# Kernel optimization log

Hardware: AMD Instinct MI355X
Metric: run time of the kernel (lower is better)

The kernel has to match this reference:

```python
import jax, jax.numpy as jnp
import numpy as np

H, DK, OUT = 8, 32, 256
SQRT_DK = float(np.sqrt(DK))


def _proj(feat, W, b):
    # (N, in) -> (N, H, DK)
    return (feat @ W + b).reshape(feat.shape[0], H, DK)


def _rel(k_src, v_src, q_dst, src, dst, att_w, msg_w, pri, n_dst):
    # HGT-style per-relation edge attention + segment softmax + aggregation.
    key = jnp.einsum('ehd,hdk->ehk', k_src[src], att_w)          # (E,H,DK)
    att = (q_dst[dst] * key).sum(-1) * pri / SQRT_DK             # (E,H)
    val = jnp.einsum('ehd,hdk->ehk', v_src[src], msg_w)          # (E,H,DK)
    m = jax.ops.segment_max(att, dst, num_segments=n_dst)
    m = jnp.where(jnp.isfinite(m), m, 0.0)
    e = jnp.exp(att - m[dst])
    s = jax.ops.segment_sum(e, dst, num_segments=n_dst)
    alpha = e / jnp.maximum(s[dst], 1e-9)
    h = jax.ops.segment_sum(alpha[..., None] * val, dst, num_segments=n_dst)
    return jax.nn.relu(h.reshape(n_dst, OUT))                    # relu per etype (reduce_func)


def _ln(x, g, b):
    mu = x.mean(-1, keepdims=True)
    var = ((x - mu) ** 2).mean(-1, keepdims=True)
    return (x - mu) / jnp.sqrt(var + 1e-5) * g + b


def _forward(feat_word, feat_topic, feat_doc, Wk, bk, Wq, bq, Wv, bv, Wa, ba,
             ln_scale, ln_bias, skip, rel_pri, rel_att, rel_msg,
             src_ww, dst_ww, src_wt, dst_wt, src_wd, dst_wd,
             src_tt, dst_tt, src_td, dst_td):
    # ntype order: word=0, topic=1, doc=2; etype order: ww=0, wt=1, wd=2, tt=3, td=4
    Nw, Nt, Nd = feat_word.shape[0], feat_topic.shape[0], feat_doc.shape[0]
    k_w, q_w, v_w = _proj(feat_word, Wk[0], bk[0]), _proj(feat_word, Wq[0], bq[0]), _proj(feat_word, Wv[0], bv[0])
    k_t, q_t, v_t = _proj(feat_topic, Wk[1], bk[1]), _proj(feat_topic, Wq[1], bq[1]), _proj(feat_topic, Wv[1], bv[1])
    q_d = _proj(feat_doc, Wq[2], bq[2])
    t_ww = _rel(k_w, v_w, q_w, src_ww, dst_ww, rel_att[0], rel_msg[0], rel_pri[0], Nw)
    t_wt = _rel(k_w, v_w, q_t, src_wt, dst_wt, rel_att[1], rel_msg[1], rel_pri[1], Nt)
    t_wd = _rel(k_w, v_w, q_d, src_wd, dst_wd, rel_att[2], rel_msg[2], rel_pri[2], Nd)
    t_tt = _rel(k_t, v_t, q_t, src_tt, dst_tt, rel_att[3], rel_msg[3], rel_pri[3], Nt)
    t_td = _rel(k_t, v_t, q_d, src_td, dst_td, rel_att[4], rel_msg[4], rel_pri[4], Nd)
    # cross_reducer='mean' across etypes targeting each ntype
    t_word, t_topic, t_doc = t_ww, (t_wt + t_tt) * 0.5, (t_wd + t_td) * 0.5
    outs = []
    for i, (t, feat) in enumerate([(t_word, feat_word), (t_topic, feat_topic), (t_doc, feat_doc)]):
        a = jax.nn.sigmoid(skip[i])
        trans = (t @ Wa[i] + ba[i]) * a + feat * (1.0 - a)
        outs.append(_ln(trans, ln_scale[i], ln_bias[i]))
    return jnp.concatenate(outs, axis=0)  # (Nw+Nt+Nd, OUT)


def setup_inputs() -> dict:
    key = jax.random.key(0)
    ks = jax.random.split(key, 32)
    Nw, Nt, Nd, D = 20000, 2000, 5000, 256
    E = {'ww': (150000, Nw, Nw), 'wt': (80000, Nw, Nt), 'wd': (80000, Nw, Nd),
         'tt': (20000, Nt, Nt), 'td': (40000, Nt, Nd)}
    inp = {
        'feat_word': jax.random.normal(ks[0], (Nw, D), jnp.float32),
        'feat_topic': jax.random.normal(ks[1], (Nt, D), jnp.float32),
        'feat_doc': jax.random.normal(ks[2], (Nd, D), jnp.float32),
        'Wk': jax.random.normal(ks[3], (3, D, D), jnp.float32) * 0.05,
        'bk': jax.random.normal(ks[4], (3, D), jnp.float32) * 0.02,
        'Wq': jax.random.normal(ks[5], (3, D, D), jnp.float32) * 0.05,
        'bq': jax.random.normal(ks[6], (3, D), jnp.float32) * 0.02,
        'Wv': jax.random.normal(ks[7], (3, D, D), jnp.float32) * 0.05,
        'bv': jax.random.normal(ks[8], (3, D), jnp.float32) * 0.02,
        'Wa': jax.random.normal(ks[9], (3, D, D), jnp.float32) * 0.05,
        'ba': jax.random.normal(ks[10], (3, D), jnp.float32) * 0.02,
        'ln_scale': jnp.ones((3, D), jnp.float32),
        'ln_bias': jnp.zeros((3, D), jnp.float32),
        'skip': jnp.ones((3,), jnp.float32),
        'rel_pri': jnp.ones((5, H), jnp.float32),
        'rel_att': jax.random.normal(ks[11], (5, H, DK, DK), jnp.float32) * 0.1,
        'rel_msg': jax.random.normal(ks[12], (5, H, DK, DK), jnp.float32) * 0.1,
    }
    for i, (et, (ne, ns, nd)) in enumerate(E.items()):
        inp['src_' + et] = jax.random.randint(ks[13 + 2 * i], (ne,), 0, ns, jnp.int32)
        inp['dst_' + et] = jax.random.randint(ks[14 + 2 * i], (ne,), 0, nd, jnp.int32)
    return inp


def reference(feat_word, feat_topic, feat_doc, Wk, bk, Wq, bq, Wv, bv, Wa, ba,
              ln_scale, ln_bias, skip, rel_pri, rel_att, rel_msg,
              src_ww, dst_ww, src_wt, dst_wt, src_wd, dst_wd,
              src_tt, dst_tt, src_td, dst_td):
    return _forward(feat_word, feat_topic, feat_doc, Wk, bk, Wq, bq, Wv, bv, Wa, ba,
                    ln_scale, ln_bias, skip, rel_pri, rel_att, rel_msg,
                    src_ww, dst_ww, src_wt, dst_wt, src_wd, dst_wd,
                    src_tt, dst_tt, src_td, dst_td)
```

## Files before the change

kernel.cpp:

```cpp
#include <hip/hip_runtime.h>

static constexpr int NW = 20000, NT = 2000, ND = 5000;
static constexpr int E_WW = 150000, E_WT = 80000, E_WD = 80000, E_TT = 20000, E_TD = 40000;

typedef short bf16x8 __attribute__((ext_vector_type(8)));
typedef float f32x4 __attribute__((ext_vector_type(4)));
typedef float f32x2 __attribute__((ext_vector_type(2)));

__device__ __forceinline__ unsigned short f2bf(float f) {
  union { float f; unsigned int u; } c; c.f = f;
  unsigned int u = c.u;
  u += 0x7fffu + ((u >> 16) & 1u);
  return (unsigned short)(u >> 16);
}
__device__ __forceinline__ float bf2f(unsigned short h) {
  union { unsigned int u; float f; } c; c.u = ((unsigned int)h) << 16; return c.f;
}
__device__ __forceinline__ bf16x8 pack8(float4 a, float4 b) {
  bf16x8 r;
  r[0] = (short)f2bf(a.x); r[1] = (short)f2bf(a.y); r[2] = (short)f2bf(a.z); r[3] = (short)f2bf(a.w);
  r[4] = (short)f2bf(b.x); r[5] = (short)f2bf(b.y); r[6] = (short)f2bf(b.z); r[7] = (short)f2bf(b.w);
  return r;
}
__device__ __forceinline__ unsigned char f2fp8(float x) {
  int p = __builtin_amdgcn_cvt_pk_fp8_f32(x, x, 0, false);
  return (unsigned char)(p & 0xff);
}

struct CsrDesc {
  const int* dst[5];
  const int* src[5];
  int E[5], N[5], cbase[5];
};

struct PrepArgs {
  const float* psrc[7]; unsigned short* pdst[7];
  const float* wq[5]; const float* bqp[5];
  unsigned short* qdst[5];
  float* beff;
  const float* att;
  const float* msg; unsigned short* wvp;
  CsrDesc dsc;
  int* counts;
  int bEff, bHw, bHist, bTot;
};
__global__ __launch_bounds__(256) void prep_kernel(PrepArgs a) {
  __shared__ float tile[32][33];
  int b = blockIdx.x;
  int tid = threadIdx.x;
  if (b < a.bEff) {
    int m = b >> 6, bk = ((b >> 3) & 7) * 32, bn = (b & 7) * 32;
    const float* W = a.psrc[m];
    unsigned short* WT = a.pdst[m];
    int tx = tid & 31, ty = tid >> 5;
#pragma unroll
    for (int i = 0; i < 32; i += 8)
      tile[ty + i][tx] = W[(size_t)(bk + ty + i) * 256 + bn + tx];
    __syncthreads();
#pragma unroll
    for (int i = 0; i < 32; i += 8)
      WT[(size_t)(bn + ty + i) * 256 + bk + tx] = f2bf(tile[tx][ty + i]);
  } else if (b < a.bHw) {
    int t = (b - a.bEff) * 256 + tid;
    if (t < 5 * 65536) {
      int r = t >> 16, rem = t & 65535;
      int n = rem >> 8, kk = rem & 255;
      int h = n >> 5, j = n & 31;
      const float* wrow = a.wq[r] + kk * 256 + h * 32;
      const float* arow = a.att + r * 8192 + h * 1024 + j * 32;
      float s = 0.f;
#pragma unroll
      for (int d = 0; d < 32; d += 4) {
        float4 wv = *(const float4*)(wrow + d);
        float4 av = *(const float4*)(arow + d);
        s += wv.x * av.x + wv.y * av.y + wv.z * av.z + wv.w * av.w;
      }
      a.qdst[r][n * 256 + kk] = f2bf(s);
    } else {
      int idx = t - 5 * 65536;
      if (idx < 1280) {
        int r = idx >> 8, n = idx & 255;
        int h = n >> 5, j = n & 31;
        const float* brow = a.bqp[r] + h * 32;
        const float* arow = a.att + r * 8192 + h * 1024 + j * 32;
        float s = 0.f;
#pragma unroll
        for (int d = 0; d < 32; d += 4) {
          float4 bv = *(const float4*)(brow + d);
          float4 av = *(const float4*)(arow + d);
          s += bv.x * av.x + bv.y * av.y + bv.z * av.z + bv.w * av.w;
        }
        a.beff[r * 256 + n] = s;
      }
    }
  } else if (b < a.bHist) {
    int t = (b - a.bHw) * 256 + tid;
    if (t < 5 * 8192) {
      int m = t >> 13, rem = t & 8191;
      int hc = rem >> 9, idx = rem & 511;
      int lane = idx >> 3, j = idx & 7;
      int h = hc >> 1, c = hc & 1;
      int k = (lane >> 4) * 8 + j, n = c * 16 + (lane & 15);
      a.wvp[t] = f2bf(a.msg[(size_t)m * 8192 + h * 1024 + k * 32 + n]);
    }
  } else {
    int t = (b - a.bHist) * 256 + tid;
    int r = 0, base = 0;
    while (r < 5 && t >= base + a.dsc.E[r]) { base += a.dsc.E[r]; r++; }
    if (r >= 5) return;
    int e = t - base;
    atomicAdd(a.counts + a.dsc.cbase[r] + a.dsc.dst[r][e], 1);
  }
}

struct ProjAll {
  const float* A[3];
  const unsigned short* WT[3];
  const float* bias[3][4];
  unsigned char* outB[3][4];
  int esz[3][4];
  int M[3], R[3], C[3], segBase[4];
  const int* counts; int* offsets; int scanN;
};
__global__ __launch_bounds__(256) void proj_all(ProjAll pa) {
  __shared__ unsigned short As[64 * 64];
  __shared__ unsigned short Bs[64 * 64];
  __shared__ int wpart2[4];
  __shared__ int carry2;
  const int tid = threadIdx.x;
  if ((int)blockIdx.x >= pa.segBase[3]) {
    int lane = tid & 63, w = tid >> 6;
    if (tid == 0) carry2 = 0;
    __syncthreads();
    const int N = pa.scanN;
    for (int base = 0; base < N; base += 1024) {
      int idx = base + tid * 4;
      int v0 = 0, v1 = 0, v2 = 0, v3 = 0;
      if (idx + 3 < N) {
        int4 t4 = *(const int4*)(pa.counts + idx);
        v0 = t4.x; v1 = t4.y; v2 = t4.z; v3 = t4.w;
      } else if (idx < N) {
        v0 = pa.counts[idx];
        if (idx + 1 < N) v1 = pa.counts[idx + 1];
        if (idx + 2 < N) v2 = pa.counts[idx + 2];
      }
      int ts = v0 + v1 + v2 + v3;
      int x = ts;
#pragma unroll
      for (int d = 1; d < 64; d <<= 1) {
        int t = __shfl_up(x, d, 64);
        if (lane >= d) x += t;
      }
      if (lane == 63) wpart2[w] = x;
      __syncthreads();
      if (tid == 0) {
        int s = 0;
#pragma unroll
        for (int j = 0; j < 4; j++) { int t = wpart2[j]; wpart2[j] = s; s += t; }
      }
      __syncthreads();
      int excl = carry2 + wpart2[w] + (x - ts);
      if (idx < N)     pa.offsets[idx]     = excl;
      if (idx + 1 < N) pa.offsets[idx + 1] = excl + v0;
      if (idx + 2 < N) pa.offsets[idx + 2] = excl + v0 + v1;
      if (idx + 3 < N) pa.offsets[idx + 3] = excl + v0 + v1 + v2;
      __syncthreads();
      if (tid == 255) carry2 = excl + ts;
      __syncthreads();
    }
    if (tid == 0) pa.offsets[N] = carry2;
    return;
  }
  int nt = 0;
  while (nt < 2 && (int)blockIdx.x >= pa.segBase[nt + 1]) nt++;
  int local = blockIdx.x - pa.segBase[nt];
  const int C = pa.C[nt];
  const int xcd = local & 7, slot = local >> 3;
  const int rt = xcd + 8 * (slot / C);
  const int bnb = slot % C;
  if (rt >= pa.R[nt]) return;
  const int bm = rt * 64, bn = bnb * 64;
  const float* A = pa.A[nt];
  const unsigned short* WT = pa.WT[nt];
  const int M = pa.M[nt];
  const int wave = tid >> 6, lane = tid & 63;
  f32x4 acc[4] = {};
  const int ar = wave * 16 + (lane & 15);
  const int swz = lane & 7;
  for (int k0 = 0; k0 < 256; k0 += 64) {
#pragma unroll
    for (int i = 0; i < 2; i++) {
      int c = tid + i * 256;
      int row = c >> 3, sl = c & 7;
      int srow = bm + row;
      float4 a0 = make_float4(0.f, 0.f, 0.f, 0.f), a1 = a0;
      if (srow < M) {
        a0 = *(const float4*)(A + (size_t)srow * 256 + k0 + sl * 8);
        a1 = *(const float4*)(A + (size_t)srow * 256 + k0 + sl * 8 + 4);
      }
      *(bf16x8*)&As[row * 64 + (sl ^ (row & 7)) * 8] = pack8(a0, a1);
      bf16x8 bv = *(const bf16x8*)(WT + (size_t)(bn + row) * 256 + k0 + sl * 8);
      *(bf16x8*)&Bs[row * 64 + (sl ^ (row & 7)) * 8] = bv;
    }
    __syncthreads();
#pragma unroll
    for (int kk = 0; kk < 2; kk++) {
      int slot2 = kk * 4 + (lane >> 4);
      bf16x8 av = *(const bf16x8*)&As[ar * 64 + ((slot2 ^ swz) * 8)];
#pragma unroll
      for (int nf = 0; nf < 4; nf++) {
        int br = nf * 16 + (lane & 15);
        bf16x8 bv = *(const bf16x8*)&Bs[br * 64 + ((slot2 ^ swz) * 8)];
        acc[nf] = __builtin_amdgcn_mfma_f32_16x16x32_bf16(av, bv, acc[nf], 0, 0, 0);
      }
    }
    __syncthreads();
  }
  const int col = lane & 15;
  const int seg = bnb >> 2;
  const float* bias = pa.bias[nt][seg];
  unsigned char* outB = pa.outB[nt][seg];
  const int esz = pa.esz[nt][seg];
  const int cbase = (bnb & 3) * 64;
#pragma unroll
  for (int nf = 0; nf < 4; nf++) {
    float bsv = bias[cbase + nf * 16 + col];
    int idx = cbase + nf * 16 + col;
#pragma unroll
    for (int rr = 0; rr < 4; rr++) {
      int row = bm + wave * 16 + (lane >> 4) * 4 + rr;
      if (row < M) {
        float v = acc[nf][rr] + bsv;
        if (esz == 2) *(unsigned short*)(outB + (size_t)row * 512 + idx * 2) = f2bf(v);
        else          outB[(size_t)row * 512 + idx] = f2fp8(v);
      }
    }
  }
}

__global__ void scatter5(CsrDesc d, const int* __restrict__ offsets, int* __restrict__ cursor,
                         int* __restrict__ ssrc) {
  int t = blockIdx.x * blockDim.x + threadIdx.x;
  int r = 0, base = 0;
  while (r < 5 && t >= base + d.E[r]) { base += d.E[r]; r++; }
  if (r >= 5) return;
  int e = t - base;
  int dn = d.dst[r][e];
  int pos = offsets[d.cbase[r] + dn] + atomicAdd(cursor + d.cbase[r] + dn, 1);
  ssrc[pos] = d.src[r][e];
}

struct AttArgs {
  const unsigned short* qh[5]; const unsigned char* kv8[5];
  const int* offs[5]; unsigned short* agg[5];
  const int* ssrc;
  const float* pri;
  int bcum[6]; int Ndst[5];
};
__global__ __launch_bounds__(256) void fused_att_agg(AttArgs a) {
  int r = 0;
  while (r < 4 && (int)blockIdx.x >= a.bcum[r + 1]) r++;
  int wave = threadIdx.x >> 6, lane = threadIdx.x & 63;
  int node = (blockIdx.x - a.bcum[r]) * 4 + wave;
  if (node >= a.Ndst[r]) return;
  const unsigned short* qh = a.qh[r];
  const unsigned char* kvb = a.kv8[r];
  const int* ssrc = a.ssrc;
  const int* offs = a.offs[r];
  int h = lane >> 3;
  float prih = a.pri[r * 8 + h] * 0.17677669529663687f;
  int r0 = offs[node], r1 = offs[node + 1];
  float4 acc = make_float4(0.f, 0.f, 0.f, 0.f);
  if (r0 < r1) {
    ushort4 qv = *(const ushort4*)(qh + (size_t)node * 256 + lane * 4);
    float q0 = bf2f(qv.x), q1 = bf2f(qv.y), q2 = bf2f(qv.z), q3 = bf2f(qv.w);
    float m = -1e30f, s = 0.f;
    for (int i = r0; i < r1; i += 2) {
      int sA = ssrc[i];
      bool two = (i + 1 < r1);
      int sB = two ? ssrc[i + 1] : sA;
      const unsigned char* pA = kvb + (size_t)sA * 512 + lane * 4;
      const unsigned char* pB = kvb + (size_t)sB * 512 + lane * 4;
      unsigned int kuA = *(const unsigned int*)pA;
      unsigned int kuB = *(const unsigned int*)pB;
      unsigned int vuA = *(const unsigned int*)(pA + 256);
      unsigned int vuB = *(const unsigned int*)(pB + 256);
      f32x2 ka01 = __builtin_amdgcn_cvt_pk_f32_fp8((int)kuA, false);
      f32x2 ka23 = __builtin_amdgcn_cvt_pk_f32_fp8((int)kuA, true);
      f32x2 kb01 = __builtin_amdgcn_cvt_pk_f32_fp8((int)kuB, false);
      f32x2 kb23 = __builtin_amdgcn_cvt_pk_f32_fp8((int)kuB, true);
      float dA = q0 * ka01[0] + q1 * ka01[1] + q2 * ka23[0] + q3 * ka23[1];
      float dB = q0 * kb01[0] + q1 * kb01[1] + q2 * kb23[0] + q3 * kb23[1];
      dA += __shfl_xor(dA, 1, 64); dB += __shfl_xor(dB, 1, 64);
      dA += __shfl_xor(dA, 2, 64); dB += __shfl_xor(dB, 2, 64);
      dA += __shfl_xor(dA, 4, 64); dB += __shfl_xor(dB, 4, 64);
      float lA = dA * prih;
      float lB = two ? dB * prih : -1e30f;
      float mn = fmaxf(m, fmaxf(lA, lB));
      float sc = __expf(m - mn);
      float wA = __expf(lA - mn);
      float wB = __expf(lB - mn);
      m = mn;
      s = s * sc + wA + wB;
      f32x2 va01 = __builtin_amdgcn_cvt_pk_f32_fp8((int)vuA, false);
      f32x2 va23 = __builtin_amdgcn_cvt_pk_f32_fp8((int)vuA, true);
      f32x2 vb01 = __builtin_amdgcn_cvt_pk_f32_fp8((int)vuB, false);
      f32x2 vb23 = __builtin_amdgcn_cvt_pk_f32_fp8((int)vuB, true);
      acc.x = acc.x * sc + wA * va01[0] + wB * vb01[0];
      acc.y = acc.y * sc + wA * va01[1] + wB * vb01[1];
      acc.z = acc.z * sc + wA * va23[0] + wB * vb23[0];
      acc.w = acc.w * sc + wA * va23[1] + wB * vb23[1];
    }
    float inv = 1.f / fmaxf(s, 1e-9f);
    acc.x *= inv; acc.y *= inv; acc.z *= inv; acc.w *= inv;
  }
  ushort4 o;
  o.x = f2bf(acc.x); o.y = f2bf(acc.y); o.z = f2bf(acc.z); o.w = f2bf(acc.w);
  *(ushort4*)(a.agg[r] + (size_t)node * 256 + lane * 4) = o;
}

struct MsgArgs {
  const unsigned short* aggA[3]; const unsigned short* aggB[3];
  const unsigned short* fA[3]; const unsigned short* fB[3];
  unsigned short* t[3];
  float scale[3];
  int N[3]; int bcum[4];
};
__global__ __launch_bounds__(256) void msg_transform_all(MsgArgs a) {
  int g = 0;
  while (g < 2 && (int)blockIdx.x >= a.bcum[g + 1]) g++;
  int local = blockIdx.x - a.bcum[g];
  const unsigned short* aggA = a.aggA[g];
  const unsigned short* aggB = a.aggB[g];
  const unsigned short* fA = a.fA[g];
  const unsigned short* fB = a.fB[g];
  unsigned short* t = a.t[g];
  float scale = a.scale[g];
  int N = a.N[g];
  int wave = threadIdx.x >> 6, lane = threadIdx.x & 63;
  int r0 = local * 64 + wave * 16;
  int arow = r0 + (lane & 15);
  bool valid = arow < N;
  int kofs = (lane >> 4) * 8;
  f32x4 z{};
#pragma unroll
  for (int h = 0; h < 8; h++) {
    bf16x8 aA{}, aB{};
    if (valid) {
      aA = *(const bf16x8*)(aggA + (size_t)arow * 256 + h * 32 + kofs);
      if (aggB) aB = *(const bf16x8*)(aggB + (size_t)arow * 256 + h * 32 + kofs);
    }
#pragma unroll
    for (int c = 0; c < 2; c++) {
      bf16x8 bA = *(const bf16x8*)(fA + ((h * 2 + c) * 64 + lane) * 8);
      f32x4 oA = __builtin_amdgcn_mfma_f32_16x16x32_bf16(aA, bA, z, 0, 0, 0);
      f32x4 oB = z;
      if (aggB) {
        bf16x8 bB = *(const bf16x8*)(fB + ((h * 2 + c) * 64 + lane) * 8);
        oB = __builtin_amdgcn_mfma_f32_16x16x32_bf16(aB, bB, z, 0, 0, 0);
      }
      int colc = h * 32 + c * 16 + (lane & 15);
#pragma unroll
      for (int rr = 0; rr < 4; rr++) {
        int row = r0 + (lane >> 4) * 4 + rr;
        if (row < N) {
          float v = fmaxf(oA[rr], 0.f) + fmaxf(oB[rr], 0.f);
          t[(size_t)row * 256 + colc] = f2bf(v * scale);
        }
      }
    }
  }
}

struct OutAll {
  const unsigned short* tA[3]; const unsigned short* WT[3];
  const float* ba[3]; const float* feat[3];
  const float* gamma[3]; const float* beta[3];
  float* op[3];
  int M[3], bcum[4];
  const float* skipv;
};
__global__ __launch_bounds__(256) void out_all_ln(OutAll oa) {
  __shared__ unsigned short As[64 * 64];
  __shared__ unsigned short Bs[256 * 64];
  int g = 0;
  while (g < 2 && (int)blockIdx.x >= oa.bcum[g + 1]) g++;
  const int bm = (blockIdx.x - oa.bcum[g]) * 64;
  const unsigned short* tA = oa.tA[g];
  const unsigned short* WT = oa.WT[g];
  const int M = oa.M[g];
  const int tid = threadIdx.x, wave = tid >> 6, lane = tid & 63;
  f32x4 acc[16] = {};
  const int ar = wave * 16 + (lane & 15);
  const int swz = lane & 7;
  for (int k0 = 0; k0 < 256; k0 += 64) {
#pragma unroll
    for (int i = 0; i < 2; i++) {
      int c = tid + i * 256;
      int row = c >> 3, sl = c & 7;
      int srow = bm + row;
      bf16x8 av{};
      if (srow < M) av = *(const bf16x8*)(tA + (size_t)srow * 256 + k0 + sl * 8);
      *(bf16x8*)&As[row * 64 + (sl ^ (row & 7)) * 8] = av;
    }
#pragma unroll
    for (int i = 0; i < 8; i++) {
      int c = tid + i * 256;
      int row = c >> 3, sl = c & 7;
      bf16x8 bv = *(const bf16x8*)(WT + (size_t)row * 256 + k0 + sl * 8);
      *(bf16x8*)&Bs[row * 64 + (sl ^ (row & 7)) * 8] = bv;
    }
    __syncthreads();
#pragma unroll
    for (int kk = 0; kk < 2; kk++) {
      int slot = kk * 4 + (lane >> 4);
      bf16x8 av = *(const bf16x8*)&As[ar * 64 + ((slot ^ swz) * 8)];
#pragma unroll
      for (int nf = 0; nf < 16; nf++) {
        int br = nf * 16 + (lane & 15);
        bf16x8 bv = *(const bf16x8*)&Bs[br * 64 + ((slot ^ swz) * 8)];
        acc[nf] = __builtin_amdgcn_mfma_f32_16x16x32_bf16(av, bv, acc[nf], 0, 0, 0);
      }
    }
    __syncthreads();
  }
  const int c16 = lane & 15;
  float a_skip = 1.f / (1.f + __expf(-oa.skipv[g]));
  float one_m = 1.f - a_skip;
  const float* gamma = oa.gamma[g];
  const float* beta = oa.beta[g];
  const float* ba = oa.ba[g];
  const float* feat = oa.feat[g];
  float* outp = oa.op[g];
  float gg[16], bb[16], bia[16];
#pragma unroll
  for (int nf = 0; nf < 16; nf++) {
    gg[nf] = gamma[nf * 16 + c16];
    bb[nf] = beta[nf * 16 + c16];
    bia[nf] = ba[nf * 16 + c16];
  }
#pragma unroll
  for (int rr = 0; rr < 4; rr++) {
    int row = bm + wave * 16 + (lane >> 4) * 4 + rr;
    bool valid = row < M;
#pragma unroll
    for (int nf = 0; nf < 16; nf++) {
      float fv = valid ? feat[(size_t)row * 256 + nf * 16 + c16] : 0.f;
      acc[nf][rr] = (acc[nf][rr] + bia[nf]) * a_skip + fv * one_m;
    }
    float p = 0.f;
#pragma unroll
    for (int nf = 0; nf < 16; nf++) p += acc[nf][rr];
    p += __shfl_xor(p, 1, 16); p += __shfl_xor(p, 2, 16);
    p += __shfl_xor(p, 4, 16); p += __shfl_xor(p, 8, 16);
    float mu = p * (1.f / 256.f);
    float qv = 0.f;
#pragma unroll
    for (int nf = 0; nf < 16; nf++) { float dd = acc[nf][rr] - mu; qv += dd * dd; }
    qv += __shfl_xor(qv, 1, 16); qv += __shfl_xor(qv, 2, 16);
    qv += __shfl_xor(qv, 4, 16); qv += __shfl_xor(qv, 8, 16);
    float rstd = rsqrtf(qv * (1.f / 256.f) + 1e-5f);
    if (valid) {
#pragma unroll
      for (int nf = 0; nf < 16; nf++)
        outp[(size_t)row * 256 + nf * 16 + c16] = (acc[nf][rr] - mu) * rstd * gg[nf] + bb[nf];
    }
  }
}

extern "C" void kernel_launch(void* const* d_in, const int* in_sizes, int n_in,
                              void* d_out, int out_size, void* d_ws, size_t ws_size,
                              hipStream_t stream) {
  const float* feat_w = (const float*)d_in[0];
  const float* feat_t = (const float*)d_in[1];
  const float* feat_d = (const float*)d_in[2];
  const float* Wk = (const float*)d_in[3];
  const float* bk = (const float*)d_in[4];
  const float* Wq = (const float*)d_in[5];
  const float* bq = (const float*)d_in[6];
  const float* Wv = (const float*)d_in[7];
  const float* bv = (const float*)d_in[8];
  const float* Wa = (const float*)d_in[9];
  const float* ba = (const float*)d_in[10];
  const float* ln_scale = (const float*)d_in[11];
  const float* ln_bias = (const float*)d_in[12];
  const float* skip = (const float*)d_in[13];
  const float* rel_pri = (const float*)d_in[14];
  const float* rel_att = (const float*)d_in[15];
  const float* rel_msg = (const float*)d_in[16];
  const int* src_ww = (const int*)d_in[17];
  const int* dst_ww = (const int*)d_in[18];
  const int* src_wt = (const int*)d_in[19];
  const int* dst_wt = (const int*)d_in[20];
  const int* src_wd = (const int*)d_in[21];
  const int* dst_wd = (const int*)d_in[22];
  const int* src_tt = (const int*)d_in[23];
  const int* dst_tt = (const int*)d_in[24];
  const int* src_td = (const int*)d_in[25];
  const int* dst_td = (const int*)d_in[26];
  float* out = (float*)d_out;
  float* ws = (float*)d_ws;

  size_t off = 0;
  auto allocF = [&](size_t nf) { float* p = ws + off; off += nf; return p; };
  unsigned char* kv_w = (unsigned char*)allocF(2560000);
  unsigned char* kv_t = (unsigned char*)allocF(256000);
  unsigned short* qhat0 = (unsigned short*)allocF(2560000);
  unsigned short* qhat1 = (unsigned short*)allocF(256000);
  unsigned short* qhat2 = (unsigned short*)allocF(640000);
  unsigned short* qhat3 = (unsigned short*)allocF(256000);
  unsigned short* qhat4 = (unsigned short*)allocF(640000);
  unsigned short* aggr0 = (unsigned short*)allocF(2560000);
  unsigned short* aggr1 = (unsigned short*)allocF(256000);
  unsigned short* aggr2 = (unsigned short*)allocF(640000);
  unsigned short* aggr3 = (unsigned short*)allocF(256000);
  unsigned short* aggr4 = (unsigned short*)allocF(640000);
  unsigned short* t_word  = (unsigned short*)allocF(2560000);
  unsigned short* t_topic = (unsigned short*)allocF(256000);
  unsigned short* t_doc   = (unsigned short*)allocF(640000);
  unsigned short* WTw = (unsigned short*)allocF(98304);
  unsigned short* WTt = (unsigned short*)allocF(131072);
  unsigned short* WTd = (unsigned short*)allocF(65536);
  unsigned short* WTa = (unsigned short*)allocF(98304);
  unsigned short* wvp = (unsigned short*)allocF(20480);
  float* bq_eff = allocF(1280);
  int* counts  = (int*)allocF(34000);
  int* cursor  = (int*)allocF(34000);
  int* offsets = (int*)allocF(34004);
  int* ssrc    = (int*)allocF(370000);

  dim3 b256(256);
  auto cdiv = [](int a, int b) { return (a + b - 1) / b; };

  CsrDesc dsc;
  dsc.dst[0] = dst_ww; dsc.dst[1] = dst_wt; dsc.dst[2] = dst_wd; dsc.dst[3] = dst_tt; dsc.dst[4] = dst_td;
  dsc.src[0] = src_ww; dsc.src[1] = src_wt; dsc.src[2] = src_wd; dsc.src[3] = src_tt; dsc.src[4] = src_td;
  int Es[5] = {E_WW, E_WT, E_WD, E_TT, E_TD};
  int Ns[5] = {NW, NT, ND, NT, ND};
  int cb = 0;
  for (int r = 0; r < 5; r++) {
    dsc.E[r] = Es[r]; dsc.N[r] = Ns[r]; dsc.cbase[r] = cb;
    cb += Ns[r];
  }

  hipMemsetAsync(counts, 0, (size_t)68000 * sizeof(int), stream);

  {
    PrepArgs pr;
    pr.psrc[0] = Wk;           pr.pdst[0] = WTw + 65536;
    pr.psrc[1] = Wv;           pr.pdst[1] = WTw + 131072;
    pr.psrc[2] = Wk + 65536;   pr.pdst[2] = WTt;
    pr.psrc[3] = Wv + 65536;   pr.pdst[3] = WTt + 65536;
    pr.psrc[4] = Wa;           pr.pdst[4] = WTa;
    pr.psrc[5] = Wa + 65536;   pr.pdst[5] = WTa + 65536;
    pr.psrc[6] = Wa + 131072;  pr.pdst[6] = WTa + 131072;
    pr.wq[0] = Wq;           pr.bqp[0] = bq;        pr.qdst[0] = WTw;
    pr.wq[1] = Wq + 65536;   pr.bqp[1] = bq + 256;  pr.qdst[1] = WTt + 131072;
    pr.wq[2] = Wq + 131072;  pr.bqp[2] = bq + 512;  pr.qdst[2] = WTd;
    pr.wq[3] = Wq + 65536;   pr.bqp[3] = bq + 256;  pr.qdst[3] = WTt + 196608;
    pr.wq[4] = Wq + 131072;  pr.bqp[4] = bq + 512;  pr.qdst[4] = WTd + 65536;
    pr.beff = bq_eff;
    pr.att = rel_att;
    pr.msg = rel_msg; pr.wvp = wvp;
    pr.dsc = dsc; pr.counts = counts;
    int nPack = 7 * 64;
    int nEff  = cdiv(5 * 65536 + 1280, 256);
    int nHw   = cdiv(5 * 8192, 256);
    int nHist = cdiv(370000, 256);
    pr.bEff  = nPack;
    pr.bHw   = nPack + nEff;
    pr.bHist = nPack + nEff + nHw;
    pr.bTot  = nPack + nEff + nHw + nHist;
    prep_kernel<<<pr.bTot, b256, 0, stream>>>(pr);
  }

  {
    ProjAll pa;
    pa.A[0] = feat_w; pa.A[1] = feat_t; pa.A[2] = feat_d;
    pa.WT[0] = WTw;   pa.WT[1] = WTt;   pa.WT[2] = WTd;
    pa.M[0] = NW; pa.M[1] = NT; pa.M[2] = ND;
    pa.bias[0][0] = bq_eff;       pa.outB[0][0] = (unsigned char*)qhat0; pa.esz[0][0] = 2;
    pa.bias[0][1] = bk;           pa.outB[0][1] = kv_w;                  pa.esz[0][1] = 1;
    pa.bias[0][2] = bv;           pa.outB[0][2] = kv_w + 256;            pa.esz[0][2] = 1;
    pa.bias[0][3] = bq_eff;       pa.outB[0][3] = (unsigned char*)qhat0; pa.esz[0][3] = 2;
    pa.bias[1][0] = bk + 256;     pa.outB[1][0] = kv_t;                  pa.esz[1][0] = 1;
    pa.bias[1][1] = bv + 256;     pa.outB[1][1] = kv_t + 256;            pa.esz[1][1] = 1;
    pa.bias[1][2] = bq_eff + 256; pa.outB[1][2] = (unsigned char*)qhat1; pa.esz[1][2] = 2;
    pa.bias[1][3] = bq_eff + 768; pa.outB[1][3] = (unsigned char*)qhat3; pa.esz[1][3] = 2;
    pa.bias[2][0] = bq_eff + 512;  pa.outB[2][0] = (unsigned char*)qhat2; pa.esz[2][0] = 2;
    pa.bias[2][1] = bq_eff + 1024; pa.outB[2][1] = (unsigned char*)qhat4; pa.esz[2][1] = 2;
    pa.bias[2][2] = bq_eff;        pa.outB[2][2] = (unsigned char*)qhat2; pa.esz[2][2] = 2;
    pa.bias[2][3] = bq_eff;        pa.outB[2][3] = (unsigned char*)qhat2; pa.esz[2][3] = 2;
    pa.R[0] = cdiv(NW, 64); pa.C[0] = 12;
    pa.R[1] = cdiv(NT, 64); pa.C[1] = 16;
    pa.R[2] = cdiv(ND, 64); pa.C[2] = 8;
    int s0 = 8 * cdiv(pa.R[0], 8) * pa.C[0];
    int s1 = 8 * cdiv(pa.R[1], 8) * pa.C[1];
    int s2 = 8 * cdiv(pa.R[2], 8) * pa.C[2];
    pa.segBase[0] = 0; pa.segBase[1] = s0; pa.segBase[2] = s0 + s1; pa.segBase[3] = s0 + s1 + s2;
    pa.counts = counts; pa.offsets = offsets; pa.scanN = 34000;
    proj_all<<<pa.segBase[3] + 1, b256, 0, stream>>>(pa);
  }

  scatter5<<<cdiv(370000, 256), b256, 0, stream>>>(dsc, offsets, cursor, ssrc);

  int NdstA[5] = {NW, NT, ND, NT, ND};

  {
    AttArgs aa;
    aa.qh[0] = qhat0; aa.qh[1] = qhat1; aa.qh[2] = qhat2; aa.qh[3] = qhat3; aa.qh[4] = qhat4;
    aa.kv8[0] = aa.kv8[1] = aa.kv8[2] = kv_w; aa.kv8[3] = aa.kv8[4] = kv_t;
    unsigned short* aggs[5] = {aggr0, aggr1, aggr2, aggr3, aggr4};
    aa.ssrc = ssrc;
    int bc = 0;
    for (int r = 0; r < 5; r++) {
      aa.offs[r] = offsets + dsc.cbase[r];
      aa.agg[r] = aggs[r];
      aa.Ndst[r] = NdstA[r];
      aa.bcum[r] = bc; bc += cdiv(NdstA[r], 4);
    }
    aa.bcum[5] = bc;
    aa.pri = rel_pri;
    fused_att_agg<<<bc, b256, 0, stream>>>(aa);
  }

  {
    MsgArgs ma;
    ma.aggA[0] = aggr0; ma.aggB[0] = nullptr;
    ma.fA[0] = wvp;             ma.fB[0] = wvp;
    ma.t[0] = t_word;  ma.scale[0] = 1.0f;  ma.N[0] = NW;
    ma.aggA[1] = aggr1; ma.aggB[1] = aggr3;
    ma.fA[1] = wvp + 8192;      ma.fB[1] = wvp + 3 * 8192;
    ma.t[1] = t_topic; ma.scale[1] = 0.5f;  ma.N[1] = NT;
    ma.aggA[2] = aggr2; ma.aggB[2] = aggr4;
    ma.fA[2] = wvp + 2 * 8192;  ma.fB[2] = wvp + 4 * 8192;
    ma.t[2] = t_doc;   ma.scale[2] = 0.5f;  ma.N[2] = ND;
    int bc = 0;
    for (int g = 0; g < 3; g++) { ma.bcum[g] = bc; bc += cdiv(ma.N[g], 64); }
    ma.bcum[3] = bc;
    msg_transform_all<<<bc, b256, 0, stream>>>(ma);
  }

  {
    OutAll oa;
    oa.tA[0] = t_word;  oa.tA[1] = t_topic; oa.tA[2] = t_doc;
    oa.WT[0] = WTa; oa.WT[1] = WTa + 65536; oa.WT[2] = WTa + 131072;
    oa.ba[0] = ba; oa.ba[1] = ba + 256; oa.ba[2] = ba + 512;
    oa.feat[0] = feat_w; oa.feat[1] = feat_t; oa.feat[2] = feat_d;
    oa.gamma[0] = ln_scale; oa.gamma[1] = ln_scale + 256; oa.gamma[2] = ln_scale + 512;
    oa.beta[0] = ln_bias; oa.beta[1] = ln_bias + 256; oa.beta[2] = ln_bias + 512;
    oa.op[0] = out; oa.op[1] = out + (size_t)NW * 256; oa.op[2] = out + (size_t)(NW + NT) * 256;
    oa.M[0] = NW; oa.M[1] = NT; oa.M[2] = ND;
    int bc = 0;
    for (int g = 0; g < 3; g++) { oa.bcum[g] = bc; bc += cdiv(oa.M[g], 64); }
    oa.bcum[3] = bc;
    oa.skipv = skip;
    out_all_ln<<<bc, b256, 0, stream>>>(oa);
  }

  (void)in_sizes; (void)n_in; (void)out_size; (void)ws_size;
}
```

Before: 196.9 us.

## Fuse message transform into output GEMM+LayerNorm kernel via shared memory

Merges the per-relation message transform (agg × rel_msg MFMA, relu, mean across etypes) into the output projection kernel. The transformed tile is written straight into a full-width 64x256 swizzled shared-memory A buffer and is never round-tripped through global memory. This removes one kernel launch and the global write and read of the t_word, t_topic and t_doc intermediates. In exchange, shared memory per block grows (A tile goes from 8KB to 32KB, 64KB total), which may lower occupancy.

```diff
diff --git a/kernel.cpp b/kernel.cpp
--- a/kernel.cpp
+++ b/kernel.cpp
@@ -319,90 +319,69 @@
   *(ushort4*)(a.agg[r] + (size_t)node * 256 + lane * 4) = o;
 }
 
-struct MsgArgs {
+struct OutAll {
   const unsigned short* aggA[3]; const unsigned short* aggB[3];
   const unsigned short* fA[3]; const unsigned short* fB[3];
-  unsigned short* t[3];
   float scale[3];
-  int N[3]; int bcum[4];
-};
-__global__ __launch_bounds__(256) void msg_transform_all(MsgArgs a) {
-  int g = 0;
-  while (g < 2 && (int)blockIdx.x >= a.bcum[g + 1]) g++;
-  int local = blockIdx.x - a.bcum[g];
-  const unsigned short* aggA = a.aggA[g];
-  const unsigned short* aggB = a.aggB[g];
-  const unsigned short* fA = a.fA[g];
-  const unsigned short* fB = a.fB[g];
-  unsigned short* t = a.t[g];
-  float scale = a.scale[g];
-  int N = a.N[g];
-  int wave = threadIdx.x >> 6, lane = threadIdx.x & 63;
-  int r0 = local * 64 + wave * 16;
-  int arow = r0 + (lane & 15);
-  bool valid = arow < N;
-  int kofs = (lane >> 4) * 8;
-  f32x4 z{};
-#pragma unroll
-  for (int h = 0; h < 8; h++) {
-    bf16x8 aA{}, aB{};
-    if (valid) {
-      aA = *(const bf16x8*)(aggA + (size_t)arow * 256 + h * 32 + kofs);
-      if (aggB) aB = *(const bf16x8*)(aggB + (size_t)arow * 256 + h * 32 + kofs);
-    }
-#pragma unroll
-    for (int c = 0; c < 2; c++) {
-      bf16x8 bA = *(const bf16x8*)(fA + ((h * 2 + c) * 64 + lane) * 8);
-      f32x4 oA = __builtin_amdgcn_mfma_f32_16x16x32_bf16(aA, bA, z, 0, 0, 0);
-      f32x4 oB = z;
-      if (aggB) {
-        bf16x8 bB = *(const bf16x8*)(fB + ((h * 2 + c) * 64 + lane) * 8);
-        oB = __builtin_amdgcn_mfma_f32_16x16x32_bf16(aB, bB, z, 0, 0, 0);
-      }
-      int colc = h * 32 + c * 16 + (lane & 15);
-#pragma unroll
-      for (int rr = 0; rr < 4; rr++) {
-        int row = r0 + (lane >> 4) * 4 + rr;
-        if (row < N) {
-          float v = fmaxf(oA[rr], 0.f) + fmaxf(oB[rr], 0.f);
-          t[(size_t)row * 256 + colc] = f2bf(v * scale);
-        }
-      }
-    }
-  }
-}
-
-struct OutAll {
-  const unsigned short* tA[3]; const unsigned short* WT[3];
+  const unsigned short* WT[3];
   const float* ba[3]; const float* feat[3];
   const float* gamma[3]; const float* beta[3];
   float* op[3];
   int M[3], bcum[4];
   const float* skipv;
 };
-__global__ __launch_bounds__(256) void out_all_ln(OutAll oa) {
-  __shared__ unsigned short As[64 * 64];
+__global__ __launch_bounds__(256) void out_all_fused(OutAll oa) {
+  __shared__ unsigned short As[64 * 256];
   __shared__ unsigned short Bs[256 * 64];
   int g = 0;
   while (g < 2 && (int)blockIdx.x >= oa.bcum[g + 1]) g++;
   const int bm = (blockIdx.x - oa.bcum[g]) * 64;
-  const unsigned short* tA = oa.tA[g];
-  const unsigned short* WT = oa.WT[g];
   const int M = oa.M[g];
   const int tid = threadIdx.x, wave = tid >> 6, lane = tid & 63;
+  {
+    const unsigned short* aggA = oa.aggA[g];
+    const unsigned short* aggB = oa.aggB[g];
+    const unsigned short* fA = oa.fA[g];
+    const unsigned short* fB = oa.fB[g];
+    const float scale = oa.scale[g];
+    int arow = bm + wave * 16 + (lane & 15);
+    bool valid = arow < M;
+    int kofs = (lane >> 4) * 8;
+    f32x4 z{};
+#pragma unroll
+    for (int h = 0; h < 8; h++) {
+      bf16x8 aA{}, aB{};
+      if (valid) {
+        aA = *(const bf16x8*)(aggA + (size_t)arow * 256 + h * 32 + kofs);
+        if (aggB) aB = *(const bf16x8*)(aggB + (size_t)arow * 256 + h * 32 + kofs);
+      }
+#pragma unroll
+      for (int c = 0; c < 2; c++) {
+        bf16x8 bA = *(const bf16x8*)(fA + ((h * 2 + c) * 64 + lane) * 8);
+        f32x4 oA = __builtin_amdgcn_mfma_f32_16x16x32_bf16(aA, bA, z, 0, 0, 0);
+        f32x4 oB = z;
+        if (aggB) {
+          bf16x8 bB = *(const bf16x8*)(fB + ((h * 2 + c) * 64 + lane) * 8);
+          oB = __builtin_amdgcn_mfma_f32_16x16x32_bf16(aB, bB, z, 0, 0, 0);
+        }
+        int colc = h * 32 + c * 16 + (lane & 15);
+        int slotc = colc >> 3, jc = colc & 7;
+#pragma unroll
+        for (int rr = 0; rr < 4; rr++) {
+          int lrow = wave * 16 + (lane >> 4) * 4 + rr;
+          float v = fmaxf(oA[rr], 0.f) + fmaxf(oB[rr], 0.f);
+          As[lrow * 256 + ((slotc ^ (lrow & 7)) * 8) + jc] = f2bf(v * scale);
+        }
+      }
+    }
+  }
+  __syncthreads();
+  const unsigned short* WT = oa.WT[g];
   f32x4 acc[16] = {};
   const int ar = wave * 16 + (lane & 15);
   const int swz = lane & 7;
   for (int k0 = 0; k0 < 256; k0 += 64) {
-#pragma unroll
-    for (int i = 0; i < 2; i++) {
-      int c = tid + i * 256;
-      int row = c >> 3, sl = c & 7;
-      int srow = bm + row;
-      bf16x8 av{};
-      if (srow < M) av = *(const bf16x8*)(tA + (size_t)srow * 256 + k0 + sl * 8);
-      *(bf16x8*)&As[row * 64 + (sl ^ (row & 7)) * 8] = av;
-    }
+    if (k0) __syncthreads();
 #pragma unroll
     for (int i = 0; i < 8; i++) {
       int c = tid + i * 256;
@@ -414,7 +393,8 @@
 #pragma unroll
     for (int kk = 0; kk < 2; kk++) {
       int slot = kk * 4 + (lane >> 4);
-      bf16x8 av = *(const bf16x8*)&As[ar * 64 + ((slot ^ swz) * 8)];
+      int gslot = (k0 >> 3) + slot;
+      bf16x8 av = *(const bf16x8*)&As[ar * 256 + ((gslot ^ swz) * 8)];
 #pragma unroll
       for (int nf = 0; nf < 16; nf++) {
         int br = nf * 16 + (lane & 15);
@@ -422,7 +402,6 @@
         acc[nf] = __builtin_amdgcn_mfma_f32_16x16x32_bf16(av, bv, acc[nf], 0, 0, 0);
       }
     }
-    __syncthreads();
   }
   const int c16 = lane & 15;
   float a_skip = 1.f / (1.f + __expf(-oa.skipv[g]));
@@ -515,9 +494,6 @@
   unsigned short* aggr2 = (unsigned short*)allocF(640000);
   unsigned short* aggr3 = (unsigned short*)allocF(256000);
   unsigned short* aggr4 = (unsigned short*)allocF(640000);
-  unsigned short* t_word  = (unsigned short*)allocF(2560000);
-  unsigned short* t_topic = (unsigned short*)allocF(256000);
-  unsigned short* t_doc   = (unsigned short*)allocF(640000);
   unsigned short* WTw = (unsigned short*)allocF(98304);
   unsigned short* WTt = (unsigned short*)allocF(131072);
   unsigned short* WTd = (unsigned short*)allocF(65536);
@@ -625,25 +601,16 @@
   }
 
   {
-    MsgArgs ma;
-    ma.aggA[0] = aggr0; ma.aggB[0] = nullptr;
-    ma.fA[0] = wvp;             ma.fB[0] = wvp;
-    ma.t[0] = t_word;  ma.scale[0] = 1.0f;  ma.N[0] = NW;
-    ma.aggA[1] = aggr1; ma.aggB[1] = aggr3;
-    ma.fA[1] = wvp + 8192;      ma.fB[1] = wvp + 3 * 8192;
-    ma.t[1] = t_topic; ma.scale[1] = 0.5f;  ma.N[1] = NT;
-    ma.aggA[2] = aggr2; ma.aggB[2] = aggr4;
-    ma.fA[2] = wvp + 2 * 8192;  ma.fB[2] = wvp + 4 * 8192;
-    ma.t[2] = t_doc;   ma.scale[2] = 0.5f;  ma.N[2] = ND;
-    int bc = 0;
-    for (int g = 0; g < 3; g++) { ma.bcum[g] = bc; bc += cdiv(ma.N[g], 64); }
-    ma.bcum[3] = bc;
-    msg_transform_all<<<bc, b256, 0, stream>>>(ma);
-  }
-
-  {
     OutAll oa;
-    oa.tA[0] = t_word;  oa.tA[1] = t_topic; oa.tA[2] = t_doc;
+    oa.aggA[0] = aggr0; oa.aggB[0] = nullptr;
+    oa.fA[0] = wvp;             oa.fB[0] = wvp;
+    oa.scale[0] = 1.0f;
+    oa.aggA[1] = aggr1; oa.aggB[1] = aggr3;
+    oa.fA[1] = wvp + 8192;      oa.fB[1] = wvp + 3 * 8192;
+    oa.scale[1] = 0.5f;
+    oa.aggA[2] = aggr2; oa.aggB[2] = aggr4;
+    oa.fA[2] = wvp + 2 * 8192;  oa.fB[2] = wvp + 4 * 8192;
+    oa.scale[2] = 0.5f;
     oa.WT[0] = WTa; oa.WT[1] = WTa + 65536; oa.WT[2] = WTa + 131072;
     oa.ba[0] = ba; oa.ba[1] = ba + 256; oa.ba[2] = ba + 512;
     oa.feat[0] = feat_w; oa.feat[1] = feat_t; oa.feat[2] = feat_d;
@@ -655,7 +622,7 @@
     for (int g = 0; g < 3; g++) { oa.bcum[g] = bc; bc += cdiv(oa.M[g], 64); }
     oa.bcum[3] = bc;
     oa.skipv = skip;
-    out_all_ln<<<bc, b256, 0, stream>>>(oa);
+    out_all_fused<<<bc, b256, 0, stream>>>(oa);
   }
 
   (void)in_sizes; (void)n_in; (void)out_size; (void)ws_size;
```

Result: faster. 183.0 us (-7.0%).
